# Optimization experiments

Hardware: AMD Instinct MI355X
Metric: run time of the kernel (lower is better)

Reference implementation:

```python
import jax, jax.numpy as jnp
import numpy as np

N = 100000      # nodes
E = 1600000     # edges (avg degree 16)
F = 16          # node input feature dim (infeat_dim1 + infeat_dim2, flag_splitfeat=False)
H = 128         # hidden_dim


def _lrelu(x, slope):
    return jnp.where(x >= 0, x, slope * x)


def setup_inputs() -> dict:
    key = jax.random.key(0)
    ks = jax.random.split(key, 16)
    feat = jax.random.normal(ks[0], (N, F), dtype=jnp.float32)
    bit_position = jax.random.uniform(ks[1], (E, 1), dtype=jnp.float32)
    src = jax.random.randint(ks[2], (E,), 0, N)
    dst = jax.random.randint(ks[3], (E,), 0, N)
    s = lambda fi, fo: 1.0 / np.sqrt(fi)
    # mlp_self: Linear(F, H//2) -> LeakyReLU(0.1) -> Linear(H//2, H)
    W_self1 = jax.random.uniform(ks[4], (F, H // 2), jnp.float32, -s(F, 0), s(F, 0))
    b_self1 = jnp.zeros((H // 2,), jnp.float32)
    W_self2 = jax.random.uniform(ks[5], (H // 2, H), jnp.float32, -s(H // 2, 0), s(H // 2, 0))
    b_self2 = jnp.zeros((H,), jnp.float32)
    # linear_neigh_module: Linear(H + F + 1, H)
    nin = H + F + 1
    W_nm = jax.random.uniform(ks[6], (nin, H), jnp.float32, -s(nin, 0), s(nin, 0))
    b_nm = jnp.zeros((H,), jnp.float32)
    # attention_vector_m: randn(H, 1)
    attn_m = jax.random.normal(ks[7], (H, 1), dtype=jnp.float32)
    # mlp_out: Linear(H, H) -> LeakyReLU(0.1) -> Linear(H, 1)
    W_out1 = jax.random.uniform(ks[8], (H, H), jnp.float32, -s(H, 0), s(H, 0))
    b_out1 = jnp.zeros((H,), jnp.float32)
    W_out2 = jax.random.uniform(ks[9], (H, 1), jnp.float32, -s(H, 0), s(H, 0))
    b_out2 = jnp.zeros((1,), jnp.float32)
    return dict(feat=feat, bit_position=bit_position, src=src, dst=dst,
                W_self1=W_self1, b_self1=b_self1, W_self2=W_self2, b_self2=b_self2,
                W_nm=W_nm, b_nm=b_nm, attn_m=attn_m,
                W_out1=W_out1, b_out1=b_out1, W_out2=W_out2, b_out2=b_out2)


def reference(feat, bit_position, src, dst,
              W_self1, b_self1, W_self2, b_self2,
              W_nm, b_nm, attn_m,
              W_out1, b_out1, W_out2, b_out2):
    n = feat.shape[0]
    # self embedding: h = mlp_self(feat)  [N, H]
    h = _lrelu(feat @ W_self1 + b_self1, 0.1) @ W_self2 + b_self2
    # edge_msg_module: z = linear_neigh_module(cat(src.h, bit_position, dst.feat))  [E, H]
    z = jnp.concatenate([h[src], bit_position, feat[dst]], axis=1) @ W_nm + b_nm
    # edge attention logits: e = LeakyReLU_0.2(z @ attn_m)  [E]
    e = _lrelu((z @ attn_m)[:, 0], 0.2)
    # per-destination softmax over incoming edges (reduce_func_attn_m)
    emax = jax.ops.segment_max(e, dst, num_segments=n)
    ee = jnp.exp(e - emax[dst])
    esum = jax.ops.segment_sum(ee, dst, num_segments=n)
    alpha = ee / esum[dst]
    # scatter-reduce weighted messages: neigh[v] = sum_e alpha_e * z_e  [N, H]
    neigh = jax.ops.segment_sum(alpha[:, None] * z, dst, num_segments=n)
    # nodes_func_module: activation has negative_slope=0 -> relu
    h_node = jnp.maximum(neigh, 0.0)
    # mlp_out: hidden -> 1
    out = _lrelu(h_node @ W_out1 + b_out1, 0.1) @ W_out2 + b_out2  # [N, 1]
    return out
```

## Files before the change

kernel.cpp:

```cpp
#include <hip/hip_runtime.h>
#include <hip/hip_fp16.h>
#include <math.h>


typedef _Float16 h2f __attribute__((ext_vector_type(2)));
typedef _Float16 h8  __attribute__((ext_vector_type(8)));
typedef float    f4  __attribute__((ext_vector_type(4)));

#define GSZ_SHIFT 6
#define GSZ 64
#define NBMAX 1664
#define EPB_H 8192
#define EPB_P1 8192
#define CAP 1536

static __device__ __forceinline__ float lrelu(float x, float s) {
    return x >= 0.f ? x : s * x;
}

__global__ void __launch_bounds__(256) k_hp(const float* __restrict__ W2,
                                            const float* __restrict__ b2,
                                            const float* __restrict__ Wnm,
                                            const float* __restrict__ b_nm,
                                            const float* __restrict__ attn,
                                            __half* __restrict__ Wc,
                                            float* __restrict__ bc,
                                            float* __restrict__ sc,
                                            const int* __restrict__ dst,
                                            int* __restrict__ bhist,
                                            int E, int NB) {
    int t = threadIdx.x;
    if (blockIdx.x == 0) {
        __shared__ float red[128];
        float m = (t < 128) ? attn[t] : 0.f;
        if (t < 128) red[t] = Wnm[128 * 128 + t] * m;
        __syncthreads();
        for (int s = 64; s > 0; s >>= 1) { if (t < s) red[t] += red[t + s]; __syncthreads(); }
        if (t == 0) sc[0] = red[0];
        __syncthreads();
        if (t < 128) red[t] = b_nm[t] * m;
        __syncthreads();
        for (int s = 64; s > 0; s >>= 1) { if (t < s) red[t] += red[t + s]; __syncthreads(); }
        if (t == 0) sc[1] = red[0];
        __syncthreads();
        for (int k = 0; k < 16; k++) {
            if (t < 128) red[t] = Wnm[(129 + k) * 128 + t] * m;
            __syncthreads();
            for (int s = 64; s > 0; s >>= 1) { if (t < s) red[t] += red[t + s]; __syncthreads(); }
            if (t == 0) sc[2 + k] = red[0];
            __syncthreads();
        }
    } else if (blockIdx.x <= 33) {
        int idx = (blockIdx.x - 1) * 256 + t;
        if (idx >= 65 * 128) return;
        int j = idx >> 7, c = idx & 127;
        const float* row = (j < 64) ? &W2[j * 128] : b2;
        float acc = 0.f;
        for (int cp = 0; cp < 128; cp++) acc = fmaf(row[cp], Wnm[cp * 128 + c], acc);
        if (j < 64) Wc[j * 128 + c] = __float2half_rn(acc);
        else bc[c] = acc;
    } else {
        __shared__ int lh[NBMAX];
        int blk = blockIdx.x - 34;
        int e0 = blk * EPB_H, e1 = min(e0 + EPB_H, E);
        for (int i = t; i < NB; i += 256) lh[i] = 0;
        __syncthreads();
        for (int e = e0 + t; e < e1; e += 256)
            atomicAdd(&lh[dst[e] >> GSZ_SHIFT], 1);
        __syncthreads();
        for (int i = t; i < NB; i += 256) {
            int c = lh[i];
            if (c) atomicAdd(&bhist[i], c);
        }
    }
}

__global__ void __launch_bounds__(256) k_Ac(const int* __restrict__ bhist,
                                            int* __restrict__ boff,
                                            int* __restrict__ bcur,
                                            const float* __restrict__ feat,
                                            const float* __restrict__ W1,
                                            const float* __restrict__ b1,
                                            const float* __restrict__ sc,
                                            const __half* __restrict__ Wc,
                                            const float* __restrict__ bc,
                                            const float* __restrict__ attn,
                                            __half* __restrict__ Ah,
                                            float* __restrict__ a_s,
                                            float* __restrict__ bd,
                                            int n, int E, int ntiles,
                                            int NB, int gridA) {
    __shared__ __half Wt[128 * 72];
    __shared__ float  W1s[16 * 64];
    __shared__ float  b1s[64];
    __shared__ __half t1s[4][16 * 72];
    int t = threadIdx.x;
    if (blockIdx.x == 0) {
        __shared__ int sd[256];
        int K = (NB + 255) >> 8;
        int loc[8];
        int b0 = t * K;
        int s = 0;
        for (int j = 0; j < K; j++) {
            int b = b0 + j;
            int c = (b < NB) ? bhist[b] : 0;
            loc[j] = s; s += c;
        }
        sd[t] = s; __syncthreads();
        for (int off = 1; off < 256; off <<= 1) {
            int x = (t >= off) ? sd[t - off] : 0;
            __syncthreads();
            sd[t] += x;
            __syncthreads();
        }
        int run = sd[t] - s;
        for (int j = 0; j < K; j++) {
            int b = b0 + j;
            if (b < NB) { int v = run + loc[j]; boff[b] = v; bcur[b] = v; }
        }
        if (t == 255) boff[NB] = sd[255];
        return;
    }
    int bid = blockIdx.x - 1;
    for (int idx = t; idx < 64 * 128; idx += 256) {
        int k = idx >> 7, c = idx & 127;
        Wt[c * 72 + k] = Wc[idx];
    }
    for (int idx = t; idx < 1024; idx += 256) W1s[idx] = W1[idx];
    if (t < 64) b1s[t] = b1[t];
    __syncthreads();
    int wave = t >> 6, lane = t & 63;
    int c = lane & 15, q = lane >> 4;
    float attv[8], bcv[8];
#pragma unroll
    for (int ct = 0; ct < 8; ct++) {
        attv[ct] = attn[ct * 16 + c];
        bcv[ct]  = bc[ct * 16 + c];
    }
    float qb[16];
#pragma unroll
    for (int k = 0; k < 16; k++) qb[k] = sc[2 + k];
    __half* myT1 = &t1s[wave][0];
    for (int tile = bid * 4 + wave; tile < ntiles; tile += gridA * 4) {
        int rowbase = tile * 16;
        int rm = min(rowbase + c, n - 1);
        const float4* fr = (const float4*)(feat + (size_t)rm * 16);
        float fv[16];
        *(float4*)&fv[0]  = fr[0];
        *(float4*)&fv[4]  = fr[1];
        *(float4*)&fv[8]  = fr[2];
        *(float4*)&fv[12] = fr[3];
        if (q == 0 && rowbase + c < n) {
            float bacc = 0.f;
#pragma unroll
            for (int k = 0; k < 16; k++) bacc = fmaf(fv[k], qb[k], bacc);
            bd[rowbase + c] = bacc;
        }
        {
            _Float16 tv[16];
#pragma unroll
            for (int jj = 0; jj < 16; jj++) {
                int j = q * 16 + jj;
                float acc = b1s[j];
#pragma unroll
                for (int k = 0; k < 16; k++) acc = fmaf(fv[k], W1s[k * 64 + j], acc);
                tv[jj] = (_Float16)lrelu(acc, 0.1f);
            }
            *(h8*)&myT1[c * 72 + q * 16 + 0] = *(h8*)&tv[0];
            *(h8*)&myT1[c * 72 + q * 16 + 8] = *(h8*)&tv[8];
        }
        h8 af[2];
#pragma unroll
        for (int ks = 0; ks < 2; ks++)
            af[ks] = *(const h8*)&myT1[c * 72 + ks * 32 + q * 8];
        f4 acc[8];
#pragma unroll
        for (int ct = 0; ct < 8; ct++) acc[ct] = (f4)(0.f);
#pragma unroll
        for (int ct = 0; ct < 8; ct++) {
#pragma unroll
            for (int ks = 0; ks < 2; ks++) {
                h8 bf = *(const h8*)&Wt[(ct * 16 + c) * 72 + ks * 32 + q * 8];
                acc[ct] = __builtin_amdgcn_mfma_f32_16x16x32_f16(af[ks], bf, acc[ct], 0, 0, 0);
            }
        }
        int rlim = n - rowbase;
        float s0 = 0.f, s1 = 0.f, s2 = 0.f, s3 = 0.f;
#pragma unroll
        for (int ct = 0; ct < 8; ct++) {
            int col = ct * 16 + c;
            float v0 = acc[ct][0] + bcv[ct];
            float v1 = acc[ct][1] + bcv[ct];
            float v2 = acc[ct][2] + bcv[ct];
            float v3 = acc[ct][3] + bcv[ct];
            if (q * 4 + 0 < rlim) Ah[(size_t)(rowbase + q * 4 + 0) * 128 + col] = __float2half_rn(v0);
            if (q * 4 + 1 < rlim) Ah[(size_t)(rowbase + q * 4 + 1) * 128 + col] = __float2half_rn(v1);
            if (q * 4 + 2 < rlim) Ah[(size_t)(rowbase + q * 4 + 2) * 128 + col] = __float2half_rn(v2);
            if (q * 4 + 3 < rlim) Ah[(size_t)(rowbase + q * 4 + 3) * 128 + col] = __float2half_rn(v3);
            s0 = fmaf(v0, attv[ct], s0);
            s1 = fmaf(v1, attv[ct], s1);
            s2 = fmaf(v2, attv[ct], s2);
            s3 = fmaf(v3, attv[ct], s3);
        }
#pragma unroll
        for (int off = 1; off < 16; off <<= 1) {
            s0 += __shfl_xor(s0, off, 64);
            s1 += __shfl_xor(s1, off, 64);
            s2 += __shfl_xor(s2, off, 64);
            s3 += __shfl_xor(s3, off, 64);
        }
        if (c == 0) {
            if (q * 4 + 0 < rlim) a_s[rowbase + q * 4 + 0] = s0;
            if (q * 4 + 1 < rlim) a_s[rowbase + q * 4 + 1] = s1;
            if (q * 4 + 2 < rlim) a_s[rowbase + q * 4 + 2] = s2;
            if (q * 4 + 3 < rlim) a_s[rowbase + q * 4 + 3] = s3;
        }
    }
}

__global__ void __launch_bounds__(512) k_p1(const int* __restrict__ src,
                                            const int* __restrict__ dst,
                                            const float* __restrict__ bit,
                                            const float* __restrict__ a_s,
                                            const float* __restrict__ bd,
                                            const float* __restrict__ sc,
                                            int* __restrict__ bcur,
                                            float4* __restrict__ tmp,
                                            int E, int NB) {
    __shared__ int hist[NBMAX];
    __shared__ int rbase[NBMAX];
    int t = threadIdx.x;
    int e0 = blockIdx.x * EPB_P1;
    int e1 = min(e0 + EPB_P1, E);
    for (int i = t; i < NB; i += 512) hist[i] = 0;
    __syncthreads();
    for (int e = e0 + t; e < e1; e += 512)
        atomicAdd(&hist[dst[e] >> GSZ_SHIFT], 1);
    __syncthreads();
    for (int i = t; i < NB; i += 512) {
        int c = hist[i];
        rbase[i] = c ? atomicAdd(&bcur[i], c) : 0;
        hist[i] = 0;
    }
    __syncthreads();
    float c1 = sc[0], c0 = sc[1];
    for (int e = e0 + t; e < e1; e += 512) {
        int s = src[e], d = dst[e];
        float bv = bit[e];
        float logit = a_s[s] + c1 * bv + bd[d] + c0;
        float w = __expf(lrelu(logit, 0.2f));
        int b = d >> GSZ_SHIFT;
        int p = rbase[b] + atomicAdd(&hist[b], 1);
        tmp[p] = make_float4(__int_as_float(s), w, w * bv, __int_as_float(d));
    }
}

__global__ void __launch_bounds__(512, 6) k_agg(const float* __restrict__ feat,
                                                const float* __restrict__ Wnm,
                                                const float* __restrict__ b_nm,
                                                const __half* __restrict__ Ah,
                                                const int* __restrict__ boff,
                                                const float4* __restrict__ tmp,
                                                __half* __restrict__ h_node,
                                                int n, int NB) {
    __shared__ float4 stg[CAP];
    __shared__ int   lcnt[GSZ], loff[GSZ], lcur[GSZ];
    __shared__ float swL[GSZ], swbL[GSZ];
    __shared__ float Wq[16 * 128];
    __shared__ float wbitL[128], bnmL[128];
    __shared__ float feats[GSZ * 16];
    int t = threadIdx.x;
    int lane = t & 63, wv = t >> 6;
    int b = blockIdx.x;
    int v0 = b << GSZ_SHIFT;
    for (int i = t; i < 16 * 128; i += 512) Wq[i] = Wnm[129 * 128 + i];
    if (t < 128) { wbitL[t] = Wnm[128 * 128 + t]; bnmL[t] = b_nm[t]; }
    for (int i = t; i < GSZ * 16; i += 512) {
        int v = v0 + (i >> 4);
        feats[i] = (v < n) ? feat[(size_t)v * 16 + (i & 15)] : 0.f;
    }
    if (t < GSZ) { swL[t] = 0.f; swbL[t] = 0.f; }
    int base = boff[b], end = boff[b + 1];
    float ax[8], ay[8];
#pragma unroll
    for (int k = 0; k < 8; k++) { ax[k] = 0.f; ay[k] = 0.f; }
    for (int c0 = base; c0 < end; c0 += CAP) {
        int cnt = min(CAP, end - c0);
        __syncthreads();
        if (t < GSZ) lcnt[t] = 0;
        __syncthreads();
        float4 r0, r1, r2;
        bool h0 = t < cnt, h1 = t + 512 < cnt, h2 = t + 1024 < cnt;
        if (h0) { r0 = tmp[c0 + t];        atomicAdd(&lcnt[__float_as_int(r0.w) & (GSZ - 1)], 1); }
        if (h1) { r1 = tmp[c0 + t + 512];  atomicAdd(&lcnt[__float_as_int(r1.w) & (GSZ - 1)], 1); }
        if (h2) { r2 = tmp[c0 + t + 1024]; atomicAdd(&lcnt[__float_as_int(r2.w) & (GSZ - 1)], 1); }
        __syncthreads();
        if (wv == 0) {
            int c = (lane < GSZ) ? lcnt[lane] : 0;
            int v = c;
#pragma unroll
            for (int d = 1; d < 64; d <<= 1) {
                int y = __shfl_up(v, d, 64);
                if (lane >= d) v += y;
            }
            if (lane < GSZ) { loff[lane] = v - c; lcur[lane] = v - c; }
        }
        __syncthreads();
        if (h0) {
            int d = __float_as_int(r0.w) & (GSZ - 1);
            stg[atomicAdd(&lcur[d], 1)] = r0;
            atomicAdd(&swL[d], r0.y); atomicAdd(&swbL[d], r0.z);
        }
        if (h1) {
            int d = __float_as_int(r1.w) & (GSZ - 1);
            stg[atomicAdd(&lcur[d], 1)] = r1;
            atomicAdd(&swL[d], r1.y); atomicAdd(&swbL[d], r1.z);
        }
        if (h2) {
            int d = __float_as_int(r2.w) & (GSZ - 1);
            stg[atomicAdd(&lcur[d], 1)] = r2;
            atomicAdd(&swL[d], r2.y); atomicAdd(&swbL[d], r2.z);
        }
        __syncthreads();
#pragma unroll
        for (int k = 0; k < 8; k++) {
            int lv = (wv << 3) + k;
            int js = loff[lv], je = js + lcnt[lv];
            float sx = 0.f, sy = 0.f;
#pragma unroll 4
            for (int j = js; j < je; j++) {
                float4 rec = stg[j];
                unsigned sv = (unsigned)__float_as_int(rec.x);
                float2 av = __half22float2(*(const __half2*)&Ah[((size_t)sv << 7) + 2 * lane]);
                sx = fmaf(rec.y, av.x, sx);
                sy = fmaf(rec.y, av.y, sy);
            }
            ax[k] += sx; ay[k] += sy;
        }
    }
    __syncthreads();
#pragma unroll
    for (int k = 0; k < 8; k++) {
        int lv = (wv << 3) + k;
        int gv = v0 + lv;
        if (gv >= n) continue;
        float swv = swL[lv];
        float hx = 0.f, hy = 0.f;
        if (swv > 0.f) {
            float inv = 1.f / swv;
            float sb = swbL[lv] * inv;
            float2 bn = *(const float2*)&bnmL[2 * lane];
            float Bx = bn.x, By = bn.y;
#pragma unroll
            for (int kk = 0; kk < 16; kk++) {
                float f = feats[lv * 16 + kk];
                float2 wq = *(const float2*)&Wq[kk * 128 + 2 * lane];
                Bx = fmaf(f, wq.x, Bx);
                By = fmaf(f, wq.y, By);
            }
            float2 wb = *(const float2*)&wbitL[2 * lane];
            hx = fmaf(sb, wb.x, ax[k] * inv) + Bx;
            hy = fmaf(sb, wb.y, ay[k] * inv) + By;
        }
        h2f o; o[0] = (_Float16)fmaxf(hx, 0.f); o[1] = (_Float16)fmaxf(hy, 0.f);
        *(h2f*)&h_node[(size_t)gv * 128 + 2 * lane] = o;
    }
}

__global__ void __launch_bounds__(256) k_out(const __half* __restrict__ h_node,
                                             const float* __restrict__ Wo1,
                                             const float* __restrict__ bo1,
                                             const float* __restrict__ Wo2,
                                             const float* __restrict__ bo2,
                                             float* __restrict__ out,
                                             int n, int ntiles) {
    __shared__ __half Wt[128 * 136];
    int t = threadIdx.x;
    for (int idx = t; idx < 128 * 128; idx += 256) {
        int k = idx >> 7, c = idx & 127;
        Wt[c * 136 + k] = __float2half_rn(Wo1[idx]);
    }
    __syncthreads();
    int wave = t >> 6, lane = t & 63;
    int c = lane & 15, q = lane >> 4;
    float b1v[8], w2v[8];
#pragma unroll
    for (int ct = 0; ct < 8; ct++) {
        b1v[ct] = bo1[ct * 16 + c];
        w2v[ct] = Wo2[ct * 16 + c];
    }
    float bias2 = bo2[0];
    for (int tile = blockIdx.x * 4 + wave; tile < ntiles; tile += gridDim.x * 4) {
        int rowbase = tile * 16;
        int rm = min(rowbase + c, n - 1);
        h8 af[4];
#pragma unroll
        for (int ks = 0; ks < 4; ks++)
            af[ks] = *(const h8*)&h_node[(size_t)rm * 128 + ks * 32 + q * 8];
        f4 acc[8];
#pragma unroll
        for (int ct = 0; ct < 8; ct++) acc[ct] = (f4)(0.f);
#pragma unroll
        for (int ct = 0; ct < 8; ct++) {
#pragma unroll
            for (int ks = 0; ks < 4; ks++) {
                h8 bf = *(const h8*)&Wt[(ct * 16 + c) * 136 + ks * 32 + q * 8];
                acc[ct] = __builtin_amdgcn_mfma_f32_16x16x32_f16(af[ks], bf, acc[ct], 0, 0, 0);
            }
        }
        int rlim = n - rowbase;
        float s0 = 0.f, s1 = 0.f, s2 = 0.f, s3 = 0.f;
#pragma unroll
        for (int ct = 0; ct < 8; ct++) {
            s0 = fmaf(lrelu(acc[ct][0] + b1v[ct], 0.1f), w2v[ct], s0);
            s1 = fmaf(lrelu(acc[ct][1] + b1v[ct], 0.1f), w2v[ct], s1);
            s2 = fmaf(lrelu(acc[ct][2] + b1v[ct], 0.1f), w2v[ct], s2);
            s3 = fmaf(lrelu(acc[ct][3] + b1v[ct], 0.1f), w2v[ct], s3);
        }
#pragma unroll
        for (int off = 1; off < 16; off <<= 1) {
            s0 += __shfl_xor(s0, off, 64);
            s1 += __shfl_xor(s1, off, 64);
            s2 += __shfl_xor(s2, off, 64);
            s3 += __shfl_xor(s3, off, 64);
        }
        if (c == 0) {
            if (q * 4 + 0 < rlim) out[rowbase + q * 4 + 0] = bias2 + s0;
            if (q * 4 + 1 < rlim) out[rowbase + q * 4 + 1] = bias2 + s1;
            if (q * 4 + 2 < rlim) out[rowbase + q * 4 + 2] = bias2 + s2;
            if (q * 4 + 3 < rlim) out[rowbase + q * 4 + 3] = bias2 + s3;
        }
    }
}

extern "C" void kernel_launch(void* const* d_in, const int* in_sizes, int n_in,
                              void* d_out, int out_size, void* d_ws, size_t ws_size,
                              hipStream_t stream) {
    const float* feat = (const float*)d_in[0];
    const float* bit  = (const float*)d_in[1];
    const int*   src  = (const int*)d_in[2];
    const int*   dst  = (const int*)d_in[3];
    const float* W1   = (const float*)d_in[4];
    const float* b1   = (const float*)d_in[5];
    const float* W2   = (const float*)d_in[6];
    const float* b2   = (const float*)d_in[7];
    const float* Wnm  = (const float*)d_in[8];
    const float* bnm  = (const float*)d_in[9];
    const float* attn = (const float*)d_in[10];
    const float* Wo1  = (const float*)d_in[11];
    const float* bo1  = (const float*)d_in[12];
    const float* Wo2  = (const float*)d_in[13];
    const float* bo2  = (const float*)d_in[14];
    float* out = (float*)d_out;
    int n = in_sizes[0] / 16;
    int E = in_sizes[2];
    int ntiles = (n + 15) / 16;
    int NB = (n + GSZ - 1) >> GSZ_SHIFT;

    char* wsp = (char*)d_ws;
    size_t off = 0;
    auto alloc = [&](size_t bytes) -> void* {
        void* p = wsp + off;
        off = (off + bytes + 255) & ~(size_t)255;
        return p;
    };
    __half* Ah       = (__half*)alloc((size_t)n * 128 * 2);
    __half* h_node   = (__half*)alloc((size_t)n * 128 * 2);
    float*  a_s      = (float*)alloc((size_t)n * 4);
    float*  bd       = (float*)alloc((size_t)n * 4);
    int*    bhist    = (int*)alloc((size_t)NBMAX * 4);
    int*    boff     = (int*)alloc((size_t)(NBMAX + 1) * 4);
    int*    bcur     = (int*)alloc((size_t)NBMAX * 4);
    float*  sc       = (float*)alloc(256);
    __half* Wc       = (__half*)alloc(64 * 128 * 2);
    float*  bc       = (float*)alloc(128 * 4);
    float4* tmp      = (float4*)alloc((size_t)E * 16);

    int gridH  = (E + EPB_H - 1) / EPB_H;
    int gridP1 = (E + EPB_P1 - 1) / EPB_P1;
    int gridA  = 1024;

    hipMemsetAsync(bhist, 0, (size_t)NB * 4, stream);
    k_hp<<<34 + gridH, 256, 0, stream>>>(W2, b2, Wnm, bnm, attn, Wc, bc, sc,
                                         dst, bhist, E, NB);
    k_Ac<<<1 + gridA, 256, 0, stream>>>(bhist, boff, bcur,
                                        feat, W1, b1, sc, Wc, bc, attn,
                                        Ah, a_s, bd, n, E, ntiles, NB, gridA);
    k_p1<<<gridP1, 512, 0, stream>>>(src, dst, bit, a_s, bd, sc, bcur, tmp, E, NB);
    k_agg<<<NB, 512, 0, stream>>>(feat, Wnm, bnm, Ah, boff, tmp, h_node, n, NB);
    k_out<<<1024, 256, 0, stream>>>(h_node, Wo1, bo1, Wo2, bo2, out, n, ntiles);
}
```

Measured before the change: 323.7 us.

## Compact edge records and move attention-weight computation into aggregation kernel

```diff
diff --git a/kernel.cpp b/kernel.cpp
--- a/kernel.cpp
+++ b/kernel.cpp
@@ -13,6 +13,7 @@
 #define EPB_H 8192
 #define EPB_P1 8192
 #define CAP 1536
+#define AGG_GRID 784
 
 static __device__ __forceinline__ float lrelu(float x, float s) {
     return x >= 0.f ? x : s * x;
@@ -221,11 +222,8 @@
 __global__ void __launch_bounds__(512) k_p1(const int* __restrict__ src,
                                             const int* __restrict__ dst,
                                             const float* __restrict__ bit,
-                                            const float* __restrict__ a_s,
-                                            const float* __restrict__ bd,
-                                            const float* __restrict__ sc,
                                             int* __restrict__ bcur,
-                                            float4* __restrict__ tmp,
+                                            int2* __restrict__ tmp,
                                             int E, int NB) {
     __shared__ int hist[NBMAX];
     __shared__ int rbase[NBMAX];
@@ -243,24 +241,23 @@
         hist[i] = 0;
     }
     __syncthreads();
-    float c1 = sc[0], c0 = sc[1];
     for (int e = e0 + t; e < e1; e += 512) {
         int s = src[e], d = dst[e];
-        float bv = bit[e];
-        float logit = a_s[s] + c1 * bv + bd[d] + c0;
-        float w = __expf(lrelu(logit, 0.2f));
         int b = d >> GSZ_SHIFT;
         int p = rbase[b] + atomicAdd(&hist[b], 1);
-        tmp[p] = make_float4(__int_as_float(s), w, w * bv, __int_as_float(d));
-    }
-}
-
-__global__ void __launch_bounds__(512, 6) k_agg(const float* __restrict__ feat,
+        tmp[p] = make_int2(s | ((d & (GSZ - 1)) << 26), __float_as_int(bit[e]));
+    }
+}
+
+__global__ void __launch_bounds__(512, 8) k_agg(const float* __restrict__ feat,
                                                 const float* __restrict__ Wnm,
                                                 const float* __restrict__ b_nm,
                                                 const __half* __restrict__ Ah,
+                                                const float* __restrict__ a_s,
+                                                const float* __restrict__ bd,
+                                                const float* __restrict__ sc,
                                                 const int* __restrict__ boff,
-                                                const float4* __restrict__ tmp,
+                                                const int2* __restrict__ tmp,
                                                 __half* __restrict__ h_node,
                                                 int n, int NB) {
     __shared__ float4 stg[CAP];
@@ -269,101 +266,129 @@
     __shared__ float Wq[16 * 128];
     __shared__ float wbitL[128], bnmL[128];
     __shared__ float feats[GSZ * 16];
+    __shared__ float bdS[GSZ];
     int t = threadIdx.x;
     int lane = t & 63, wv = t >> 6;
-    int b = blockIdx.x;
-    int v0 = b << GSZ_SHIFT;
     for (int i = t; i < 16 * 128; i += 512) Wq[i] = Wnm[129 * 128 + i];
     if (t < 128) { wbitL[t] = Wnm[128 * 128 + t]; bnmL[t] = b_nm[t]; }
-    for (int i = t; i < GSZ * 16; i += 512) {
-        int v = v0 + (i >> 4);
-        feats[i] = (v < n) ? feat[(size_t)v * 16 + (i & 15)] : 0.f;
-    }
-    if (t < GSZ) { swL[t] = 0.f; swbL[t] = 0.f; }
-    int base = boff[b], end = boff[b + 1];
-    float ax[8], ay[8];
-#pragma unroll
-    for (int k = 0; k < 8; k++) { ax[k] = 0.f; ay[k] = 0.f; }
-    for (int c0 = base; c0 < end; c0 += CAP) {
-        int cnt = min(CAP, end - c0);
-        __syncthreads();
-        if (t < GSZ) lcnt[t] = 0;
-        __syncthreads();
-        float4 r0, r1, r2;
-        bool h0 = t < cnt, h1 = t + 512 < cnt, h2 = t + 1024 < cnt;
-        if (h0) { r0 = tmp[c0 + t];        atomicAdd(&lcnt[__float_as_int(r0.w) & (GSZ - 1)], 1); }
-        if (h1) { r1 = tmp[c0 + t + 512];  atomicAdd(&lcnt[__float_as_int(r1.w) & (GSZ - 1)], 1); }
-        if (h2) { r2 = tmp[c0 + t + 1024]; atomicAdd(&lcnt[__float_as_int(r2.w) & (GSZ - 1)], 1); }
-        __syncthreads();
-        if (wv == 0) {
-            int c = (lane < GSZ) ? lcnt[lane] : 0;
-            int v = c;
-#pragma unroll
-            for (int d = 1; d < 64; d <<= 1) {
-                int y = __shfl_up(v, d, 64);
-                if (lane >= d) v += y;
-            }
-            if (lane < GSZ) { loff[lane] = v - c; lcur[lane] = v - c; }
-        }
-        __syncthreads();
-        if (h0) {
-            int d = __float_as_int(r0.w) & (GSZ - 1);
-            stg[atomicAdd(&lcur[d], 1)] = r0;
-            atomicAdd(&swL[d], r0.y); atomicAdd(&swbL[d], r0.z);
-        }
-        if (h1) {
-            int d = __float_as_int(r1.w) & (GSZ - 1);
-            stg[atomicAdd(&lcur[d], 1)] = r1;
-            atomicAdd(&swL[d], r1.y); atomicAdd(&swbL[d], r1.z);
-        }
-        if (h2) {
-            int d = __float_as_int(r2.w) & (GSZ - 1);
-            stg[atomicAdd(&lcur[d], 1)] = r2;
-            atomicAdd(&swL[d], r2.y); atomicAdd(&swbL[d], r2.z);
-        }
-        __syncthreads();
+    float c1s = sc[0], c0s = sc[1];
+    for (int b = blockIdx.x; b < NB; b += gridDim.x) {
+        int v0 = b << GSZ_SHIFT;
+        __syncthreads();
+        for (int i = t; i < GSZ * 16; i += 512) {
+            int v = v0 + (i >> 4);
+            feats[i] = (v < n) ? feat[(size_t)v * 16 + (i & 15)] : 0.f;
+        }
+        if (t < GSZ) {
+            int v = v0 + t;
+            bdS[t] = (v < n) ? bd[v] : 0.f;
+            swL[t] = 0.f; swbL[t] = 0.f;
+        }
+        int base = boff[b], end = boff[b + 1];
+        float ax[8], ay[8];
+#pragma unroll
+        for (int k = 0; k < 8; k++) { ax[k] = 0.f; ay[k] = 0.f; }
+        for (int cb = base; cb < end; cb += CAP) {
+            int cnt = min(CAP, end - cb);
+            __syncthreads();
+            if (t < GSZ) lcnt[t] = 0;
+            __syncthreads();
+            float4 r0, r1, r2;
+            bool h0 = t < cnt, h1 = t + 512 < cnt, h2 = t + 1024 < cnt;
+            if (h0) {
+                int2 e = tmp[cb + t];
+                int s = e.x & 0x03FFFFFF, dl = (unsigned)e.x >> 26;
+                float bv = __int_as_float(e.y);
+                float w = __expf(lrelu(a_s[s] + c1s * bv + bdS[dl] + c0s, 0.2f));
+                r0 = make_float4(__int_as_float(s), w, w * bv, __int_as_float(dl));
+                atomicAdd(&lcnt[dl], 1);
+            }
+            if (h1) {
+                int2 e = tmp[cb + t + 512];
+                int s = e.x & 0x03FFFFFF, dl = (unsigned)e.x >> 26;
+                float bv = __int_as_float(e.y);
+                float w = __expf(lrelu(a_s[s] + c1s * bv + bdS[dl] + c0s, 0.2f));
+                r1 = make_float4(__int_as_float(s), w, w * bv, __int_as_float(dl));
+                atomicAdd(&lcnt[dl], 1);
+            }
+            if (h2) {
+                int2 e = tmp[cb + t + 1024];
+                int s = e.x & 0x03FFFFFF, dl = (unsigned)e.x >> 26;
+                float bv = __int_as_float(e.y);
+                float w = __expf(lrelu(a_s[s] + c1s * bv + bdS[dl] + c0s, 0.2f));
+                r2 = make_float4(__int_as_float(s), w, w * bv, __int_as_float(dl));
+                atomicAdd(&lcnt[dl], 1);
+            }
+            __syncthreads();
+            if (wv == 0) {
+                int c = lcnt[lane];
+                int v = c;
+#pragma unroll
+                for (int d = 1; d < 64; d <<= 1) {
+                    int y = __shfl_up(v, d, 64);
+                    if (lane >= d) v += y;
+                }
+                loff[lane] = v - c; lcur[lane] = v - c;
+            }
+            __syncthreads();
+            if (h0) {
+                int dl = __float_as_int(r0.w);
+                stg[atomicAdd(&lcur[dl], 1)] = r0;
+                atomicAdd(&swL[dl], r0.y); atomicAdd(&swbL[dl], r0.z);
+            }
+            if (h1) {
+                int dl = __float_as_int(r1.w);
+                stg[atomicAdd(&lcur[dl], 1)] = r1;
+                atomicAdd(&swL[dl], r1.y); atomicAdd(&swbL[dl], r1.z);
+            }
+            if (h2) {
+                int dl = __float_as_int(r2.w);
+                stg[atomicAdd(&lcur[dl], 1)] = r2;
+                atomicAdd(&swL[dl], r2.y); atomicAdd(&swbL[dl], r2.z);
+            }
+            __syncthreads();
+#pragma unroll
+            for (int k = 0; k < 8; k++) {
+                int lv = (k << 3) | wv;
+                int js = loff[lv], je = js + lcnt[lv];
+                float sx = 0.f, sy = 0.f;
+#pragma unroll 8
+                for (int j = js; j < je; j++) {
+                    float4 rec = stg[j];
+                    unsigned sv = (unsigned)__float_as_int(rec.x);
+                    float2 av = __half22float2(*(const __half2*)&Ah[((size_t)sv << 7) + 2 * lane]);
+                    sx = fmaf(rec.y, av.x, sx);
+                    sy = fmaf(rec.y, av.y, sy);
+                }
+                ax[k] += sx; ay[k] += sy;
+            }
+        }
 #pragma unroll
         for (int k = 0; k < 8; k++) {
-            int lv = (wv << 3) + k;
-            int js = loff[lv], je = js + lcnt[lv];
-            float sx = 0.f, sy = 0.f;
-#pragma unroll 4
-            for (int j = js; j < je; j++) {
-                float4 rec = stg[j];
-                unsigned sv = (unsigned)__float_as_int(rec.x);
-                float2 av = __half22float2(*(const __half2*)&Ah[((size_t)sv << 7) + 2 * lane]);
-                sx = fmaf(rec.y, av.x, sx);
-                sy = fmaf(rec.y, av.y, sy);
-            }
-            ax[k] += sx; ay[k] += sy;
-        }
-    }
-    __syncthreads();
-#pragma unroll
-    for (int k = 0; k < 8; k++) {
-        int lv = (wv << 3) + k;
-        int gv = v0 + lv;
-        if (gv >= n) continue;
-        float swv = swL[lv];
-        float hx = 0.f, hy = 0.f;
-        if (swv > 0.f) {
-            float inv = 1.f / swv;
-            float sb = swbL[lv] * inv;
-            float2 bn = *(const float2*)&bnmL[2 * lane];
-            float Bx = bn.x, By = bn.y;
-#pragma unroll
-            for (int kk = 0; kk < 16; kk++) {
-                float f = feats[lv * 16 + kk];
-                float2 wq = *(const float2*)&Wq[kk * 128 + 2 * lane];
-                Bx = fmaf(f, wq.x, Bx);
-                By = fmaf(f, wq.y, By);
-            }
-            float2 wb = *(const float2*)&wbitL[2 * lane];
-            hx = fmaf(sb, wb.x, ax[k] * inv) + Bx;
-            hy = fmaf(sb, wb.y, ay[k] * inv) + By;
-        }
-        h2f o; o[0] = (_Float16)fmaxf(hx, 0.f); o[1] = (_Float16)fmaxf(hy, 0.f);
-        *(h2f*)&h_node[(size_t)gv * 128 + 2 * lane] = o;
+            int lv = (k << 3) | wv;
+            int gv = v0 + lv;
+            if (gv >= n) continue;
+            float swv = swL[lv];
+            float hx = 0.f, hy = 0.f;
+            if (swv > 0.f) {
+                float inv = 1.f / swv;
+                float sb = swbL[lv] * inv;
+                float2 bn = *(const float2*)&bnmL[2 * lane];
+                float Bx = bn.x, By = bn.y;
+#pragma unroll
+                for (int kk = 0; kk < 16; kk++) {
+                    float f = feats[lv * 16 + kk];
+                    float2 wq = *(const float2*)&Wq[kk * 128 + 2 * lane];
+                    Bx = fmaf(f, wq.x, Bx);
+                    By = fmaf(f, wq.y, By);
+                }
+                float2 wb = *(const float2*)&wbitL[2 * lane];
+                hx = fmaf(sb, wb.x, ax[k] * inv) + Bx;
+                hy = fmaf(sb, wb.y, ay[k] * inv) + By;
+            }
+            h2f o; o[0] = (_Float16)fmaxf(hx, 0.f); o[1] = (_Float16)fmaxf(hy, 0.f);
+            *(h2f*)&h_node[(size_t)gv * 128 + 2 * lane] = o;
+        }
     }
 }
 
@@ -474,11 +499,12 @@
     float*  sc       = (float*)alloc(256);
     __half* Wc       = (__half*)alloc(64 * 128 * 2);
     float*  bc       = (float*)alloc(128 * 4);
-    float4* tmp      = (float4*)alloc((size_t)E * 16);
+    int2*   tmp      = (int2*)alloc((size_t)E * 8);
 
     int gridH  = (E + EPB_H - 1) / EPB_H;
     int gridP1 = (E + EPB_P1 - 1) / EPB_P1;
     int gridA  = 1024;
+    int gridAg = (NB < AGG_GRID) ? NB : AGG_GRID;
 
     hipMemsetAsync(bhist, 0, (size_t)NB * 4, stream);
     k_hp<<<34 + gridH, 256, 0, stream>>>(W2, b2, Wnm, bnm, attn, Wc, bc, sc,
@@ -486,7 +512,8 @@
     k_Ac<<<1 + gridA, 256, 0, stream>>>(bhist, boff, bcur,
                                         feat, W1, b1, sc, Wc, bc, attn,
                                         Ah, a_s, bd, n, E, ntiles, NB, gridA);
-    k_p1<<<gridP1, 512, 0, stream>>>(src, dst, bit, a_s, bd, sc, bcur, tmp, E, NB);
-    k_agg<<<NB, 512, 0, stream>>>(feat, Wnm, bnm, Ah, boff, tmp, h_node, n, NB);
+    k_p1<<<gridP1, 512, 0, stream>>>(src, dst, bit, bcur, tmp, E, NB);
+    k_agg<<<gridAg, 512, 0, stream>>>(feat, Wnm, bnm, Ah, a_s, bd, sc,
+                                      boff, tmp, h_node, n, NB);
     k_out<<<1024, 256, 0, stream>>>(h_node, Wo1, bo1, Wo2, bo2, out, n, ntiles);
 }
```

Result: slower. 343.0 us (+5.9%).

## Make aggregation kernel persistent with atomic work queue and slimmer staging

Applied to the files above, without the earlier changes.

```diff
diff --git a/kernel.cpp b/kernel.cpp
--- a/kernel.cpp
+++ b/kernel.cpp
@@ -13,6 +13,7 @@
 #define EPB_H 8192
 #define EPB_P1 8192
 #define CAP 1536
+#define AGG_GRID 1024
 
 static __device__ __forceinline__ float lrelu(float x, float s) {
     return x >= 0.f ? x : s * x;
@@ -78,6 +79,7 @@
 __global__ void __launch_bounds__(256) k_Ac(const int* __restrict__ bhist,
                                             int* __restrict__ boff,
                                             int* __restrict__ bcur,
+                                            int* __restrict__ wcur,
                                             const float* __restrict__ feat,
                                             const float* __restrict__ W1,
                                             const float* __restrict__ b1,
@@ -89,7 +91,7 @@
                                             float* __restrict__ a_s,
                                             float* __restrict__ bd,
                                             int n, int E, int ntiles,
-                                            int NB, int gridA) {
+                                            int NB, int gridA, int gridAg) {
     __shared__ __half Wt[128 * 72];
     __shared__ float  W1s[16 * 64];
     __shared__ float  b1s[64];
@@ -119,6 +121,7 @@
             if (b < NB) { int v = run + loc[j]; boff[b] = v; bcur[b] = v; }
         }
         if (t == 255) boff[NB] = sd[255];
+        if (t == 0) wcur[0] = gridAg;
         return;
     }
     int bid = blockIdx.x - 1;
@@ -261,109 +264,116 @@
                                                 const __half* __restrict__ Ah,
                                                 const int* __restrict__ boff,
                                                 const float4* __restrict__ tmp,
+                                                int* __restrict__ wcur,
                                                 __half* __restrict__ h_node,
                                                 int n, int NB) {
-    __shared__ float4 stg[CAP];
+    __shared__ float2 stg[CAP];
     __shared__ int   lcnt[GSZ], loff[GSZ], lcur[GSZ];
     __shared__ float swL[GSZ], swbL[GSZ];
     __shared__ float Wq[16 * 128];
     __shared__ float wbitL[128], bnmL[128];
     __shared__ float feats[GSZ * 16];
+    __shared__ int   bnext;
     int t = threadIdx.x;
     int lane = t & 63, wv = t >> 6;
-    int b = blockIdx.x;
-    int v0 = b << GSZ_SHIFT;
     for (int i = t; i < 16 * 128; i += 512) Wq[i] = Wnm[129 * 128 + i];
     if (t < 128) { wbitL[t] = Wnm[128 * 128 + t]; bnmL[t] = b_nm[t]; }
-    for (int i = t; i < GSZ * 16; i += 512) {
-        int v = v0 + (i >> 4);
-        feats[i] = (v < n) ? feat[(size_t)v * 16 + (i & 15)] : 0.f;
-    }
-    if (t < GSZ) { swL[t] = 0.f; swbL[t] = 0.f; }
-    int base = boff[b], end = boff[b + 1];
-    float ax[8], ay[8];
-#pragma unroll
-    for (int k = 0; k < 8; k++) { ax[k] = 0.f; ay[k] = 0.f; }
-    for (int c0 = base; c0 < end; c0 += CAP) {
-        int cnt = min(CAP, end - c0);
-        __syncthreads();
-        if (t < GSZ) lcnt[t] = 0;
-        __syncthreads();
-        float4 r0, r1, r2;
-        bool h0 = t < cnt, h1 = t + 512 < cnt, h2 = t + 1024 < cnt;
-        if (h0) { r0 = tmp[c0 + t];        atomicAdd(&lcnt[__float_as_int(r0.w) & (GSZ - 1)], 1); }
-        if (h1) { r1 = tmp[c0 + t + 512];  atomicAdd(&lcnt[__float_as_int(r1.w) & (GSZ - 1)], 1); }
-        if (h2) { r2 = tmp[c0 + t + 1024]; atomicAdd(&lcnt[__float_as_int(r2.w) & (GSZ - 1)], 1); }
-        __syncthreads();
-        if (wv == 0) {
-            int c = (lane < GSZ) ? lcnt[lane] : 0;
-            int v = c;
-#pragma unroll
-            for (int d = 1; d < 64; d <<= 1) {
-                int y = __shfl_up(v, d, 64);
-                if (lane >= d) v += y;
-            }
-            if (lane < GSZ) { loff[lane] = v - c; lcur[lane] = v - c; }
-        }
-        __syncthreads();
-        if (h0) {
-            int d = __float_as_int(r0.w) & (GSZ - 1);
-            stg[atomicAdd(&lcur[d], 1)] = r0;
-            atomicAdd(&swL[d], r0.y); atomicAdd(&swbL[d], r0.z);
-        }
-        if (h1) {
-            int d = __float_as_int(r1.w) & (GSZ - 1);
-            stg[atomicAdd(&lcur[d], 1)] = r1;
-            atomicAdd(&swL[d], r1.y); atomicAdd(&swbL[d], r1.z);
-        }
-        if (h2) {
-            int d = __float_as_int(r2.w) & (GSZ - 1);
-            stg[atomicAdd(&lcur[d], 1)] = r2;
-            atomicAdd(&swL[d], r2.y); atomicAdd(&swbL[d], r2.z);
-        }
-        __syncthreads();
+    int b = blockIdx.x;
+    while (b < NB) {
+        int v0 = b << GSZ_SHIFT;
+        __syncthreads();
+        for (int i = t; i < GSZ * 16; i += 512) {
+            int v = v0 + (i >> 4);
+            feats[i] = (v < n) ? feat[(size_t)v * 16 + (i & 15)] : 0.f;
+        }
+        if (t < GSZ) { swL[t] = 0.f; swbL[t] = 0.f; }
+        if (t == 0) bnext = atomicAdd(wcur, 1);
+        int base = boff[b], end = boff[b + 1];
+        float ax[8], ay[8];
+#pragma unroll
+        for (int k = 0; k < 8; k++) { ax[k] = 0.f; ay[k] = 0.f; }
+        for (int cb = base; cb < end; cb += CAP) {
+            int cnt = min(CAP, end - cb);
+            __syncthreads();
+            if (t < GSZ) lcnt[t] = 0;
+            __syncthreads();
+            float4 r0, r1, r2;
+            bool h0 = t < cnt, h1 = t + 512 < cnt, h2 = t + 1024 < cnt;
+            if (h0) { r0 = tmp[cb + t];        atomicAdd(&lcnt[__float_as_int(r0.w) & (GSZ - 1)], 1); }
+            if (h1) { r1 = tmp[cb + t + 512];  atomicAdd(&lcnt[__float_as_int(r1.w) & (GSZ - 1)], 1); }
+            if (h2) { r2 = tmp[cb + t + 1024]; atomicAdd(&lcnt[__float_as_int(r2.w) & (GSZ - 1)], 1); }
+            __syncthreads();
+            if (wv == 0) {
+                int c = lcnt[lane];
+                int v = c;
+#pragma unroll
+                for (int d = 1; d < 64; d <<= 1) {
+                    int y = __shfl_up(v, d, 64);
+                    if (lane >= d) v += y;
+                }
+                loff[lane] = v - c; lcur[lane] = v - c;
+            }
+            __syncthreads();
+            if (h0) {
+                int dl = __float_as_int(r0.w) & (GSZ - 1);
+                stg[atomicAdd(&lcur[dl], 1)] = make_float2(r0.x, r0.y);
+                atomicAdd(&swL[dl], r0.y); atomicAdd(&swbL[dl], r0.z);
+            }
+            if (h1) {
+                int dl = __float_as_int(r1.w) & (GSZ - 1);
+                stg[atomicAdd(&lcur[dl], 1)] = make_float2(r1.x, r1.y);
+                atomicAdd(&swL[dl], r1.y); atomicAdd(&swbL[dl], r1.z);
+            }
+            if (h2) {
+                int dl = __float_as_int(r2.w) & (GSZ - 1);
+                stg[atomicAdd(&lcur[dl], 1)] = make_float2(r2.x, r2.y);
+                atomicAdd(&swL[dl], r2.y); atomicAdd(&swbL[dl], r2.z);
+            }
+            __syncthreads();
+#pragma unroll
+            for (int k = 0; k < 8; k++) {
+                int lv = (k << 3) | wv;
+                int js = loff[lv], je = js + lcnt[lv];
+                float sx = 0.f, sy = 0.f;
+#pragma unroll 8
+                for (int j = js; j < je; j++) {
+                    float2 rec = stg[j];
+                    unsigned sv = (unsigned)__float_as_int(rec.x);
+                    float2 av = __half22float2(*(const __half2*)&Ah[((size_t)sv << 7) + 2 * lane]);
+                    sx = fmaf(rec.y, av.x, sx);
+                    sy = fmaf(rec.y, av.y, sy);
+                }
+                ax[k] += sx; ay[k] += sy;
+            }
+        }
 #pragma unroll
         for (int k = 0; k < 8; k++) {
-            int lv = (wv << 3) + k;
-            int js = loff[lv], je = js + lcnt[lv];
-            float sx = 0.f, sy = 0.f;
-#pragma unroll 4
-            for (int j = js; j < je; j++) {
-                float4 rec = stg[j];
-                unsigned sv = (unsigned)__float_as_int(rec.x);
-                float2 av = __half22float2(*(const __half2*)&Ah[((size_t)sv << 7) + 2 * lane]);
-                sx = fmaf(rec.y, av.x, sx);
-                sy = fmaf(rec.y, av.y, sy);
-            }
-            ax[k] += sx; ay[k] += sy;
-        }
-    }
-    __syncthreads();
-#pragma unroll
-    for (int k = 0; k < 8; k++) {
-        int lv = (wv << 3) + k;
-        int gv = v0 + lv;
-        if (gv >= n) continue;
-        float swv = swL[lv];
-        float hx = 0.f, hy = 0.f;
-        if (swv > 0.f) {
-            float inv = 1.f / swv;
-            float sb = swbL[lv] * inv;
-            float2 bn = *(const float2*)&bnmL[2 * lane];
-            float Bx = bn.x, By = bn.y;
-#pragma unroll
-            for (int kk = 0; kk < 16; kk++) {
-                float f = feats[lv * 16 + kk];
-                float2 wq = *(const float2*)&Wq[kk * 128 + 2 * lane];
-                Bx = fmaf(f, wq.x, Bx);
-                By = fmaf(f, wq.y, By);
-            }
-            float2 wb = *(const float2*)&wbitL[2 * lane];
-            hx = fmaf(sb, wb.x, ax[k] * inv) + Bx;
-            hy = fmaf(sb, wb.y, ay[k] * inv) + By;
-        }
-        h2f o; o[0] = (_Float16)fmaxf(hx, 0.f); o[1] = (_Float16)fmaxf(hy, 0.f);
-        *(h2f*)&h_node[(size_t)gv * 128 + 2 * lane] = o;
+            int lv = (k << 3) | wv;
+            int gv = v0 + lv;
+            if (gv >= n) continue;
+            float swv = swL[lv];
+            float hx = 0.f, hy = 0.f;
+            if (swv > 0.f) {
+                float inv = 1.f / swv;
+                float sb = swbL[lv] * inv;
+                float2 bn = *(const float2*)&bnmL[2 * lane];
+                float Bx = bn.x, By = bn.y;
+#pragma unroll
+                for (int kk = 0; kk < 16; kk++) {
+                    float f = feats[lv * 16 + kk];
+                    float2 wq = *(const float2*)&Wq[kk * 128 + 2 * lane];
+                    Bx = fmaf(f, wq.x, Bx);
+                    By = fmaf(f, wq.y, By);
+                }
+                float2 wb = *(const float2*)&wbitL[2 * lane];
+                hx = fmaf(sb, wb.x, ax[k] * inv) + Bx;
+                hy = fmaf(sb, wb.y, ay[k] * inv) + By;
+            }
+            h2f o; o[0] = (_Float16)fmaxf(hx, 0.f); o[1] = (_Float16)fmaxf(hy, 0.f);
+            *(h2f*)&h_node[(size_t)gv * 128 + 2 * lane] = o;
+        }
+        __syncthreads();
+        b = bnext;
     }
 }
 
@@ -471,6 +481,7 @@
     int*    bhist    = (int*)alloc((size_t)NBMAX * 4);
     int*    boff     = (int*)alloc((size_t)(NBMAX + 1) * 4);
     int*    bcur     = (int*)alloc((size_t)NBMAX * 4);
+    int*    wcur     = (int*)alloc(256);
     float*  sc       = (float*)alloc(256);
     __half* Wc       = (__half*)alloc(64 * 128 * 2);
     float*  bc       = (float*)alloc(128 * 4);
@@ -479,14 +490,16 @@
     int gridH  = (E + EPB_H - 1) / EPB_H;
     int gridP1 = (E + EPB_P1 - 1) / EPB_P1;
     int gridA  = 1024;
+    int gridAg = (NB < AGG_GRID) ? NB : AGG_GRID;
 
     hipMemsetAsync(bhist, 0, (size_t)NB * 4, stream);
     k_hp<<<34 + gridH, 256, 0, stream>>>(W2, b2, Wnm, bnm, attn, Wc, bc, sc,
                                          dst, bhist, E, NB);
-    k_Ac<<<1 + gridA, 256, 0, stream>>>(bhist, boff, bcur,
+    k_Ac<<<1 + gridA, 256, 0, stream>>>(bhist, boff, bcur, wcur,
                                         feat, W1, b1, sc, Wc, bc, attn,
-                                        Ah, a_s, bd, n, E, ntiles, NB, gridA);
+                                        Ah, a_s, bd, n, E, ntiles, NB, gridA, gridAg);
     k_p1<<<gridP1, 512, 0, stream>>>(src, dst, bit, a_s, bd, sc, bcur, tmp, E, NB);
-    k_agg<<<NB, 512, 0, stream>>>(feat, Wnm, bnm, Ah, boff, tmp, h_node, n, NB);
+    k_agg<<<gridAg, 512, 0, stream>>>(feat, Wnm, bnm, Ah, boff, tmp, wcur,
+                                      h_node, n, NB);
     k_out<<<1024, 256, 0, stream>>>(h_node, Wo1, bo1, Wo2, bo2, out, n, ntiles);
 }
```

Result: slower. 377.0 us (+16.5%).

## Precompute per-node edge ranks in binning pass to drop the per-chunk local sort in aggregation

Applied to the files above, without the earlier changes.

```diff
diff --git a/kernel.cpp b/kernel.cpp
--- a/kernel.cpp
+++ b/kernel.cpp
@@ -12,7 +12,7 @@
 #define NBMAX 1664
 #define EPB_H 8192
 #define EPB_P1 8192
-#define CAP 1536
+#define CAP 1344
 
 static __device__ __forceinline__ float lrelu(float x, float s) {
     return x >= 0.f ? x : s * x;
@@ -225,6 +225,7 @@
                                             const float* __restrict__ bd,
                                             const float* __restrict__ sc,
                                             int* __restrict__ bcur,
+                                            int* __restrict__ ncur,
                                             float4* __restrict__ tmp,
                                             int E, int NB) {
     __shared__ int hist[NBMAX];
@@ -251,7 +252,9 @@
         float w = __expf(lrelu(logit, 0.2f));
         int b = d >> GSZ_SHIFT;
         int p = rbase[b] + atomicAdd(&hist[b], 1);
-        tmp[p] = make_float4(__int_as_float(s), w, w * bv, __int_as_float(d));
+        int rank = atomicAdd(&ncur[d], 1);
+        int packed = ((d & (GSZ - 1)) << 7) | rank;
+        tmp[p] = make_float4(__int_as_float(s), w, w * bv, __int_as_float(packed));
     }
 }
 
@@ -260,12 +263,13 @@
                                                 const float* __restrict__ b_nm,
                                                 const __half* __restrict__ Ah,
                                                 const int* __restrict__ boff,
+                                                const int* __restrict__ ncur,
                                                 const float4* __restrict__ tmp,
                                                 __half* __restrict__ h_node,
                                                 int n, int NB) {
-    __shared__ float4 stg[CAP];
-    __shared__ int   lcnt[GSZ], loff[GSZ], lcur[GSZ];
-    __shared__ float swL[GSZ], swbL[GSZ];
+    __shared__ float2 stgA[CAP];
+    __shared__ float  stgB[CAP];
+    __shared__ int   lcnt[GSZ], loffS[GSZ];
     __shared__ float Wq[16 * 128];
     __shared__ float wbitL[128], bnmL[128];
     __shared__ float feats[GSZ * 16];
@@ -279,76 +283,70 @@
         int v = v0 + (i >> 4);
         feats[i] = (v < n) ? feat[(size_t)v * 16 + (i & 15)] : 0.f;
     }
-    if (t < GSZ) { swL[t] = 0.f; swbL[t] = 0.f; }
+    if (wv == 0) {
+        int v = v0 + lane;
+        int c = (v < n) ? ncur[v] : 0;
+        lcnt[lane] = c;
+        int p = c;
+#pragma unroll
+        for (int d = 1; d < 64; d <<= 1) {
+            int y = __shfl_up(p, d, 64);
+            if (lane >= d) p += y;
+        }
+        loffS[lane] = p - c;
+    }
     int base = boff[b], end = boff[b + 1];
-    float ax[8], ay[8];
-#pragma unroll
-    for (int k = 0; k < 8; k++) { ax[k] = 0.f; ay[k] = 0.f; }
-    for (int c0 = base; c0 < end; c0 += CAP) {
-        int cnt = min(CAP, end - c0);
-        __syncthreads();
-        if (t < GSZ) lcnt[t] = 0;
-        __syncthreads();
-        float4 r0, r1, r2;
-        bool h0 = t < cnt, h1 = t + 512 < cnt, h2 = t + 1024 < cnt;
-        if (h0) { r0 = tmp[c0 + t];        atomicAdd(&lcnt[__float_as_int(r0.w) & (GSZ - 1)], 1); }
-        if (h1) { r1 = tmp[c0 + t + 512];  atomicAdd(&lcnt[__float_as_int(r1.w) & (GSZ - 1)], 1); }
-        if (h2) { r2 = tmp[c0 + t + 1024]; atomicAdd(&lcnt[__float_as_int(r2.w) & (GSZ - 1)], 1); }
-        __syncthreads();
-        if (wv == 0) {
-            int c = (lane < GSZ) ? lcnt[lane] : 0;
-            int v = c;
-#pragma unroll
-            for (int d = 1; d < 64; d <<= 1) {
-                int y = __shfl_up(v, d, 64);
-                if (lane >= d) v += y;
-            }
-            if (lane < GSZ) { loff[lane] = v - c; lcur[lane] = v - c; }
-        }
-        __syncthreads();
-        if (h0) {
-            int d = __float_as_int(r0.w) & (GSZ - 1);
-            stg[atomicAdd(&lcur[d], 1)] = r0;
-            atomicAdd(&swL[d], r0.y); atomicAdd(&swbL[d], r0.z);
-        }
-        if (h1) {
-            int d = __float_as_int(r1.w) & (GSZ - 1);
-            stg[atomicAdd(&lcur[d], 1)] = r1;
-            atomicAdd(&swL[d], r1.y); atomicAdd(&swbL[d], r1.z);
-        }
-        if (h2) {
-            int d = __float_as_int(r2.w) & (GSZ - 1);
-            stg[atomicAdd(&lcur[d], 1)] = r2;
-            atomicAdd(&swL[d], r2.y); atomicAdd(&swbL[d], r2.z);
-        }
-        __syncthreads();
-#pragma unroll
-        for (int k = 0; k < 8; k++) {
-            int lv = (wv << 3) + k;
-            int js = loff[lv], je = js + lcnt[lv];
-            float sx = 0.f, sy = 0.f;
-#pragma unroll 4
-            for (int j = js; j < je; j++) {
-                float4 rec = stg[j];
-                unsigned sv = (unsigned)__float_as_int(rec.x);
-                float2 av = __half22float2(*(const __half2*)&Ah[((size_t)sv << 7) + 2 * lane]);
-                sx = fmaf(rec.y, av.x, sx);
-                sy = fmaf(rec.y, av.y, sy);
-            }
-            ax[k] += sx; ay[k] += sy;
-        }
-    }
-    __syncthreads();
+    int cnt = end - base;
+    float4 r0, r1, r2;
+    bool h0 = t < cnt, h1 = t + 512 < cnt, h2 = t + 1024 < cnt;
+    if (h0) r0 = tmp[base + t];
+    if (h1) r1 = tmp[base + t + 512];
+    if (h2) r2 = tmp[base + t + 1024];
+    __syncthreads();
+    if (h0) {
+        int p = __float_as_int(r0.w);
+        int slot = loffS[p >> 7] + (p & 127);
+        stgA[slot] = make_float2(r0.x, r0.y); stgB[slot] = r0.z;
+    }
+    if (h1) {
+        int p = __float_as_int(r1.w);
+        int slot = loffS[p >> 7] + (p & 127);
+        stgA[slot] = make_float2(r1.x, r1.y); stgB[slot] = r1.z;
+    }
+    if (h2) {
+        int p = __float_as_int(r2.w);
+        int slot = loffS[p >> 7] + (p & 127);
+        stgA[slot] = make_float2(r2.x, r2.y); stgB[slot] = r2.z;
+    }
+    __syncthreads();
+    float ax[8], ay[8], swr[8], sbr[8];
 #pragma unroll
     for (int k = 0; k < 8; k++) {
-        int lv = (wv << 3) + k;
+        int lv = (k << 3) | wv;
+        int js = loffS[lv], je = js + lcnt[lv];
+        float sx = 0.f, sy = 0.f, sw = 0.f, sb = 0.f;
+#pragma unroll 8
+        for (int j = js; j < je; j++) {
+            float2 rec = stgA[j];
+            unsigned sv = (unsigned)__float_as_int(rec.x);
+            float2 av = __half22float2(*(const __half2*)&Ah[((size_t)sv << 7) + 2 * lane]);
+            sx = fmaf(rec.y, av.x, sx);
+            sy = fmaf(rec.y, av.y, sy);
+            sw += rec.y;
+            sb += stgB[j];
+        }
+        ax[k] = sx; ay[k] = sy; swr[k] = sw; sbr[k] = sb;
+    }
+#pragma unroll
+    for (int k = 0; k < 8; k++) {
+        int lv = (k << 3) | wv;
         int gv = v0 + lv;
         if (gv >= n) continue;
-        float swv = swL[lv];
+        float swv = swr[k];
         float hx = 0.f, hy = 0.f;
         if (swv > 0.f) {
             float inv = 1.f / swv;
-            float sb = swbL[lv] * inv;
+            float sb = sbr[k] * inv;
             float2 bn = *(const float2*)&bnmL[2 * lane];
             float Bx = bn.x, By = bn.y;
 #pragma unroll
@@ -471,6 +469,7 @@
     int*    bhist    = (int*)alloc((size_t)NBMAX * 4);
     int*    boff     = (int*)alloc((size_t)(NBMAX + 1) * 4);
     int*    bcur     = (int*)alloc((size_t)NBMAX * 4);
+    int*    ncur     = (int*)alloc((size_t)n * 4);
     float*  sc       = (float*)alloc(256);
     __half* Wc       = (__half*)alloc(64 * 128 * 2);
     float*  bc       = (float*)alloc(128 * 4);
@@ -481,12 +480,15 @@
     int gridA  = 1024;
 
     hipMemsetAsync(bhist, 0, (size_t)NB * 4, stream);
+    hipMemsetAsync(ncur, 0, (size_t)n * 4, stream);
     k_hp<<<34 + gridH, 256, 0, stream>>>(W2, b2, Wnm, bnm, attn, Wc, bc, sc,
                                          dst, bhist, E, NB);
     k_Ac<<<1 + gridA, 256, 0, stream>>>(bhist, boff, bcur,
                                         feat, W1, b1, sc, Wc, bc, attn,
                                         Ah, a_s, bd, n, E, ntiles, NB, gridA);
-    k_p1<<<gridP1, 512, 0, stream>>>(src, dst, bit, a_s, bd, sc, bcur, tmp, E, NB);
-    k_agg<<<NB, 512, 0, stream>>>(feat, Wnm, bnm, Ah, boff, tmp, h_node, n, NB);
+    k_p1<<<gridP1, 512, 0, stream>>>(src, dst, bit, a_s, bd, sc, bcur, ncur,
+                                     tmp, E, NB);
+    k_agg<<<NB, 512, 0, stream>>>(feat, Wnm, bnm, Ah, boff, ncur, tmp,
+                                  h_node, n, NB);
     k_out<<<1024, 256, 0, stream>>>(h_node, Wo1, bo1, Wo2, bo2, out, n, ntiles);
 }
```

New measurement: 344.8 us. 6.5% more time.
